# Optimization experiments

Hardware: AMD Instinct MI355X
Metric: run time of the kernel (lower is better)

Reference implementation:

```python
import jax, jax.numpy as jnp
import numpy as np

B, S, D, H = 2, 2048, 1024, 16
HEAD_DIM = D // H  # 64


def setup_inputs() -> dict:
    key = jax.random.key(0)
    ks = jax.random.split(key, 7)
    x = jax.random.normal(ks[0], (B, S, D), dtype=jnp.float32)
    W_q = jax.random.normal(ks[1], (D, D), dtype=jnp.float32) * 0.02
    W_k = jax.random.normal(ks[2], (D, D), dtype=jnp.float32) * 0.02
    W_v = jax.random.normal(ks[3], (D, D), dtype=jnp.float32) * 0.02
    W_o = jax.random.normal(ks[4], (D, D), dtype=jnp.float32) * 0.02 / np.sqrt(2 * 12)
    b_o = jnp.zeros((D,), dtype=jnp.float32)
    # Ragged prefix attention_mask: per-row valid lengths in [S/2, S];
    # row 0 forced to full length so max_valid_len == S statically (jit-safe).
    lengths = jax.random.randint(ks[5], (B,), S // 2, S + 1)
    lengths = lengths.at[0].set(S)
    attention_mask = (jnp.arange(S)[None, :] < lengths[:, None]).astype(jnp.float32)
    return {"x": x, "attention_mask": attention_mask, "W_q": W_q, "W_k": W_k,
            "W_v": W_v, "W_o": W_o, "b_o": b_o}


def reference(x, attention_mask, W_q, W_k, W_v, W_o, b_o):
    b, s, d = x.shape
    h, hd = H, HEAD_DIM
    # QKV projections (no bias, qkv_bias=False)
    q = (x @ W_q.T).reshape(b, s, h, hd).transpose(0, 2, 1, 3)  # [b,h,s,hd]
    # Masking keys/values at invalid (padded) positions; for prefix masks this
    # is exactly the module's per-batch packing loop (max_valid_len == s).
    m = attention_mask[:, None, :, None]  # [b,1,s,1]
    k = ((x @ W_k.T).reshape(b, s, h, hd).transpose(0, 2, 1, 3)) * m
    v = ((x @ W_v.T).reshape(b, s, h, hd).transpose(0, 2, 1, 3)) * m
    # Naive causal attention, same op order as the torch module:
    # mask with -inf first, then scale by 1/sqrt(head_dim), then softmax.
    causal = jnp.triu(jnp.ones((s, s), dtype=bool), 1)  # True above diagonal
    scores = jnp.einsum('bhqd,bhkd->bhqk', q, k)
    scores = jnp.where(causal[None, None], -jnp.inf, scores)
    att = jax.nn.softmax(scores / jnp.sqrt(jnp.float32(hd)), axis=-1)
    ctx = jnp.einsum('bhqk,bhkd->bhqd', att, v)  # [b,h,s,hd]
    ctx = ctx.transpose(0, 2, 1, 3).reshape(b, s, d)
    # Output projection (dropout is inference no-op)
    return ctx @ W_o.T + b_o
```

## Files before the change

### kernel.cpp

```cpp
#include <hip/hip_runtime.h>

#define B_  2
#define S_  2048
#define D_  1024
#define H_  16
#define HD_ 64
#define N3_ 3072
#define M_  4096

typedef _Float16 f16;
typedef _Float16 f16x2 __attribute__((ext_vector_type(2)));
typedef _Float16 f16x4 __attribute__((ext_vector_type(4)));
typedef _Float16 f16x8 __attribute__((ext_vector_type(8)));
typedef float    f32x4 __attribute__((ext_vector_type(4)));

__device__ __forceinline__ void async16(const f16* g, f16* l) {
  __builtin_amdgcn_global_load_lds(
      (const __attribute__((address_space(1))) unsigned int*)g,
      (__attribute__((address_space(3))) unsigned int*)l, 16, 0, 0);
}

__device__ __forceinline__ f16x2 pkrtz(float a, float b) {
  return __builtin_bit_cast(f16x2, __builtin_amdgcn_cvt_pkrtz(a, b));
}

__device__ __forceinline__ float vexp2(float x) {
  float r; asm("v_exp_f32 %0, %1" : "=v"(r) : "v"(x)); return r;
}

__global__ __launch_bounds__(256)
void cvt_all(const float* __restrict__ x,
             const float* __restrict__ Wq, const float* __restrict__ Wk,
             const float* __restrict__ Wv, const float* __restrict__ Wo,
             f16* __restrict__ xb, f16* __restrict__ wdst, float qscale) {
  const int i = blockIdx.x * 256 + threadIdx.x;
  const int XN4 = M_ * D_ / 4;
  const int WN4 = D_ * D_ / 4;
  const float* src;
  f16* dst;
  float scale = 1.0f;
  int j;
  if (i < XN4) {
    src = x; dst = xb; j = i;
  } else {
    int k = i - XN4;
    int m = k >> 18;
    j = k & (WN4 - 1);
    src = (m == 0) ? Wq : (m == 1) ? Wk : (m == 2) ? Wv : Wo;
    if (m == 0) scale = qscale;
    dst = wdst + (size_t)m * D_ * D_;
  }
  float4 v = ((const float4*)src)[j];
  f16x4 o = { (f16)(v.x * scale), (f16)(v.y * scale),
              (f16)(v.z * scale), (f16)(v.w * scale) };
  ((f16x4*)dst)[j] = o;
}

__global__ __launch_bounds__(256)
void gemm_qkv(const f16* __restrict__ A, const f16* __restrict__ Bw,
              f16* __restrict__ Cq, f16* __restrict__ vtout,
              const float* __restrict__ mask) {
  __shared__ f16 As0[64 * 64];
  __shared__ f16 Bs0[128 * 64];
  __shared__ f16 As1[64 * 64];
  __shared__ f16 Bs1[128 * 64];

  const int tid  = threadIdx.x;
  const int lane = tid & 63;
  const int w    = tid >> 6;
  const int lcol = lane & 15;
  const int quad = lane >> 4;
  const int lx   = lcol & 7;
  const int wave_m = w >> 1, wave_n = w & 1;

  const int lin  = blockIdx.x;
  const int xcd  = lin & 7;
  const int c    = lin >> 3;
  const int mIdx = c / 12;
  const int nIdx = c - mIdx * 12;
  const int m0 = ((xcd >> 1) * 16 + mIdx) * 64;
  const int n0 = ((xcd & 1) * 12 + nIdx) * 128;

  const int rr  = lane >> 3;
  const int gch = (lane & 7) ^ rr;

  const f16* gA[2];
  const f16* gB[4];
#pragma unroll
  for (int i = 0; i < 2; i++) {
    int seg = 2 * w + i;
    gA[i] = A + (size_t)(m0 + seg * 8 + rr) * D_ + gch * 8;
  }
#pragma unroll
  for (int i = 0; i < 4; i++) {
    int seg = i * 4 + w;
    gB[i] = Bw + (size_t)(n0 + seg * 8 + rr) * D_ + gch * 8;
  }

  int offA[2], offB[4];
#pragma unroll
  for (int i = 0; i < 2; i++) offA[i] = (wave_m * 32 + i * 16 + lcol) * 64;
#pragma unroll
  for (int i = 0; i < 4; i++) offB[i] = (wave_n * 64 + i * 16 + lcol) * 64;

  const f32x4 zero = {0.f, 0.f, 0.f, 0.f};
  f32x4 acc[2][4];
#pragma unroll
  for (int i = 0; i < 2; i++)
#pragma unroll
    for (int j = 0; j < 4; j++) acc[i][j] = zero;

  auto stage = [&](int k0, f16* sA, f16* sB) {
#pragma unroll
    for (int i = 0; i < 2; i++) async16(gA[i] + k0, sA + (2 * w + i) * 512);
#pragma unroll
    for (int i = 0; i < 4; i++) async16(gB[i] + k0, sB + (i * 4 + w) * 512);
  };
  auto compute = [&](const f16* sA, const f16* sB) {
#pragma unroll
    for (int ks = 0; ks < 2; ks++) {
      const int co = ((quad + 4 * ks) ^ lx) * 8;
      f16x8 af[2], bf[4];
#pragma unroll
      for (int i = 0; i < 2; i++) af[i] = *(const f16x8*)(sA + offA[i] + co);
#pragma unroll
      for (int i = 0; i < 4; i++) bf[i] = *(const f16x8*)(sB + offB[i] + co);
#pragma unroll
      for (int mi = 0; mi < 2; mi++)
#pragma unroll
        for (int ni = 0; ni < 4; ni++)
          acc[mi][ni] = __builtin_amdgcn_mfma_f32_16x16x32_f16(
              af[mi], bf[ni], acc[mi][ni], 0, 0, 0);
    }
  };

  stage(0, As0, Bs0);
  for (int it = 0; it < 14; it += 2) {
    stage((it + 1) * 64, As1, Bs1);
    asm volatile("s_waitcnt vmcnt(6)\ns_barrier" ::: "memory");
    compute(As0, Bs0);
    asm volatile("s_barrier" ::: "memory");
    stage((it + 2) * 64, As0, Bs0);
    asm volatile("s_waitcnt vmcnt(6)\ns_barrier" ::: "memory");
    compute(As1, Bs1);
    asm volatile("s_barrier" ::: "memory");
  }
  stage(15 * 64, As1, Bs1);
  asm volatile("s_waitcnt vmcnt(6)\ns_barrier" ::: "memory");
  compute(As0, Bs0);
  asm volatile("s_waitcnt vmcnt(0)\ns_barrier" ::: "memory");
  compute(As1, Bs1);

#pragma unroll
  for (int mi = 0; mi < 2; mi++) {
    const int mgb = m0 + wave_m * 32 + mi * 16 + quad * 4;
    const int bb = mgb >> 11, s = mgb & (S_ - 1);
    const float mk0 = mask[mgb], mk1 = mask[mgb + 1];
    const float mk2 = mask[mgb + 2], mk3 = mask[mgb + 3];
    const float mks[4] = {mk0, mk1, mk2, mk3};
    if (n0 >= 2 * D_) {
#pragma unroll
      for (int ni = 0; ni < 4; ni++) {
        const int vcol = n0 - 2 * D_ + wave_n * 64 + ni * 16 + lcol;
        f16x4 v = { (f16)(acc[mi][ni][0] * mk0), (f16)(acc[mi][ni][1] * mk1),
                    (f16)(acc[mi][ni][2] * mk2), (f16)(acc[mi][ni][3] * mk3) };
        *(f16x4*)(vtout +
                  ((size_t)(bb * 16 + (vcol >> 6)) * 64 + (vcol & 63)) * S_ + s) = v;
      }
    } else {
      const bool kmask = (n0 >= D_);
#pragma unroll
      for (int r = 0; r < 4; r++) {
        const float mk = kmask ? mks[r] : 1.0f;
#pragma unroll
        for (int ni = 0; ni < 4; ni++) {
          int ng = n0 + wave_n * 64 + ni * 16 + lcol;
          Cq[(size_t)(mgb + r) * N3_ + ng] = (f16)(acc[mi][ni][r] * mk);
        }
      }
    }
  }
}

__global__ __launch_bounds__(256)
void gemm_proj(const f16* __restrict__ A, const f16* __restrict__ Bw,
               float* __restrict__ Cf, const float* __restrict__ bias) {
  __shared__ f16 As0[64 * 64];
  __shared__ f16 Bs0[128 * 64];
  __shared__ f16 As1[64 * 64];
  __shared__ f16 Bs1[128 * 64];

  const int tid  = threadIdx.x;
  const int lane = tid & 63;
  const int w    = tid >> 6;
  const int lcol = lane & 15;
  const int quad = lane >> 4;
  const int lx   = lcol & 7;
  const int wave_m = w >> 1, wave_n = w & 1;

  const int lin  = blockIdx.x;
  const int xcd  = lin & 7;
  const int c    = lin >> 3;
  const int mIdx = c >> 2;
  const int nIdx = c & 3;
  const int m0 = ((xcd >> 1) * 16 + mIdx) * 64;
  const int n0 = ((xcd & 1) * 4 + nIdx) * 128;

  const int rr  = lane >> 3;
  const int gch = (lane & 7) ^ rr;

  const f16* gA[2];
  const f16* gB[4];
#pragma unroll
  for (int i = 0; i < 2; i++) {
    int seg = 2 * w + i;
    gA[i] = A + (size_t)(m0 + seg * 8 + rr) * D_ + gch * 8;
  }
#pragma unroll
  for (int i = 0; i < 4; i++) {
    int seg = i * 4 + w;
    gB[i] = Bw + (size_t)(n0 + seg * 8 + rr) * D_ + gch * 8;
  }

  int offA[2], offB[4];
#pragma unroll
  for (int i = 0; i < 2; i++) offA[i] = (wave_m * 32 + i * 16 + lcol) * 64;
#pragma unroll
  for (int i = 0; i < 4; i++) offB[i] = (wave_n * 64 + i * 16 + lcol) * 64;

  const f32x4 zero = {0.f, 0.f, 0.f, 0.f};
  f32x4 acc[2][4];
#pragma unroll
  for (int i = 0; i < 2; i++)
#pragma unroll
    for (int j = 0; j < 4; j++) acc[i][j] = zero;

  auto stage = [&](int k0, f16* sA, f16* sB) {
#pragma unroll
    for (int i = 0; i < 2; i++) async16(gA[i] + k0, sA + (2 * w + i) * 512);
#pragma unroll
    for (int i = 0; i < 4; i++) async16(gB[i] + k0, sB + (i * 4 + w) * 512);
  };
  auto compute = [&](const f16* sA, const f16* sB) {
#pragma unroll
    for (int ks = 0; ks < 2; ks++) {
      const int co = ((quad + 4 * ks) ^ lx) * 8;
      f16x8 af[2], bf[4];
#pragma unroll
      for (int i = 0; i < 2; i++) af[i] = *(const f16x8*)(sA + offA[i] + co);
#pragma unroll
      for (int i = 0; i < 4; i++) bf[i] = *(const f16x8*)(sB + offB[i] + co);
#pragma unroll
      for (int mi = 0; mi < 2; mi++)
#pragma unroll
        for (int ni = 0; ni < 4; ni++)
          acc[mi][ni] = __builtin_amdgcn_mfma_f32_16x16x32_f16(
              af[mi], bf[ni], acc[mi][ni], 0, 0, 0);
    }
  };

  stage(0, As0, Bs0);
  for (int it = 0; it < 14; it += 2) {
    stage((it + 1) * 64, As1, Bs1);
    asm volatile("s_waitcnt vmcnt(6)\ns_barrier" ::: "memory");
    compute(As0, Bs0);
    asm volatile("s_barrier" ::: "memory");
    stage((it + 2) * 64, As0, Bs0);
    asm volatile("s_waitcnt vmcnt(6)\ns_barrier" ::: "memory");
    compute(As1, Bs1);
    asm volatile("s_barrier" ::: "memory");
  }
  stage(15 * 64, As1, Bs1);
  asm volatile("s_waitcnt vmcnt(6)\ns_barrier" ::: "memory");
  compute(As0, Bs0);
  asm volatile("s_waitcnt vmcnt(0)\ns_barrier" ::: "memory");
  compute(As1, Bs1);

#pragma unroll
  for (int mi = 0; mi < 2; mi++) {
#pragma unroll
    for (int r = 0; r < 4; r++) {
      int mg = m0 + wave_m * 32 + mi * 16 + quad * 4 + r;
#pragma unroll
      for (int ni = 0; ni < 4; ni++) {
        int ng = n0 + wave_n * 64 + ni * 16 + lcol;
        Cf[(size_t)mg * D_ + ng] = acc[mi][ni][r] + bias[ng];
      }
    }
  }
}

__global__ __launch_bounds__(128)
void flash_attn8(const f16* __restrict__ qkv, const f16* __restrict__ vt,
                 f16* __restrict__ ctx, float* __restrict__ part) {
  __shared__ f16 Ks[64 * 64];
  __shared__ f16 Vs[64 * 64];

  const int tid  = threadIdx.x;
  const int lane = tid & 63;
  const int w    = tid >> 6;
  const int lcol = lane & 15;
  const int quad = lane >> 4;
  const int lx   = lcol & 7;

  const int id   = blockIdx.x;
  const int bh   = (id & 7) + 8 * ((id >> 3) & 3);
  const int u    = id >> 5;
  const int p    = u & 15;
  const int role = u >> 4;
  const int g    = 31 - p;
  const int b    = bh >> 4, h = bh & 15;

  const int rsub = lane >> 3;
  const int gch  = (lane & 7) ^ rsub;
  const f16* Kg = qkv + (size_t)b * S_ * N3_ + D_ + h * HD_;
  const f16* Vg = vt + (size_t)bh * HD_ * S_;

  int srow[4];
  f16 *ldsK[4], *ldsV[4];
#pragma unroll
  for (int i = 0; i < 4; i++) {
    const int r0 = w * 32 + i * 8;
    srow[i] = r0 + rsub;
    ldsK[i] = Ks + r0 * 64;
    ldsV[i] = Vs + r0 * 64;
  }

  const f32x4 zero = {0.f, 0.f, 0.f, 0.f};
  f32x4 o0[4], o1[4];
  float lp0, lp1;

  auto run = [&](int qt, int ktb, int kte) {
    const int qrow0 = qt * 64 + w * 32 + lcol;
    const int qrow1 = qrow0 + 16;
    const f16* Qp0 = qkv + (size_t)(b * S_ + qrow0) * N3_ + h * HD_;
    const f16* Qp1 = qkv + (size_t)(b * S_ + qrow1) * N3_ + h * HD_;
    const f16x8 qa0 = *(const f16x8*)(Qp0 + quad * 8);
    const f16x8 qa1 = *(const f16x8*)(Qp0 + 32 + quad * 8);
    const f16x8 qb0 = *(const f16x8*)(Qp1 + quad * 8);
    const f16x8 qb1 = *(const f16x8*)(Qp1 + 32 + quad * 8);
#pragma unroll
    for (int i = 0; i < 4; i++) { o0[i] = zero; o1[i] = zero; }
    lp0 = 0.f; lp1 = 0.f;

    for (int kt = ktb; kt < kte; kt++) {
      const int kbase = kt * 64;
      __syncthreads();
#pragma unroll
      for (int i = 0; i < 4; i++)
        async16(Kg + (size_t)(kbase + srow[i]) * N3_ + gch * 8, ldsK[i]);
#pragma unroll
      for (int i = 0; i < 4; i++)
        async16(Vg + (size_t)srow[i] * S_ + kbase + gch * 8, ldsV[i]);
      __syncthreads();

      f32x4 sc0[4], sc1[4];
#pragma unroll
      for (int ct = 0; ct < 4; ct++) {
        const f16* kr = Ks + (ct * 16 + lcol) * 64;
        f16x8 kf0 = *(const f16x8*)(kr + ((quad    ) ^ lx) * 8);
        f16x8 kf1 = *(const f16x8*)(kr + ((quad + 4) ^ lx) * 8);
        f32x4 z0 = zero;
        z0 = __builtin_amdgcn_mfma_f32_16x16x32_f16(kf0, qa0, z0, 0, 0, 0);
        z0 = __builtin_amdgcn_mfma_f32_16x16x32_f16(kf1, qa1, z0, 0, 0, 0);
        sc0[ct] = z0;
        f32x4 z1 = zero;
        z1 = __builtin_amdgcn_mfma_f32_16x16x32_f16(kf0, qb0, z1, 0, 0, 0);
        z1 = __builtin_amdgcn_mfma_f32_16x16x32_f16(kf1, qb1, z1, 0, 0, 0);
        sc1[ct] = z1;
      }

      if (kt == qt) {
        const int qoff0 = w * 32 + lcol;
        const int qoff1 = qoff0 + 16;
#pragma unroll
        for (int ct = 0; ct < 4; ct++) {
          const int koff = ct * 16 + quad * 4;
#pragma unroll
          for (int r = 0; r < 4; r++) {
            if (koff + r > qoff0) sc0[ct][r] = -1e30f;
            if (koff + r > qoff1) sc1[ct][r] = -1e30f;
          }
        }
      }

      f16x4 pf0[4], pf1[4];
#pragma unroll
      for (int ct = 0; ct < 4; ct++) {
        float a0 = vexp2(sc0[ct][0]), a1 = vexp2(sc0[ct][1]);
        float a2 = vexp2(sc0[ct][2]), a3 = vexp2(sc0[ct][3]);
        lp0 += (a0 + a1) + (a2 + a3);
        f16x2 alo = pkrtz(a0, a1);
        f16x2 ahi = pkrtz(a2, a3);
        f16x4 pa = { alo[0], alo[1], ahi[0], ahi[1] };
        pf0[ct] = pa;
        float b0 = vexp2(sc1[ct][0]), b1 = vexp2(sc1[ct][1]);
        float b2 = vexp2(sc1[ct][2]), b3 = vexp2(sc1[ct][3]);
        lp1 += (b0 + b1) + (b2 + b3);
        f16x2 blo = pkrtz(b0, b1);
        f16x2 bhi = pkrtz(b2, b3);
        f16x4 pb = { blo[0], blo[1], bhi[0], bhi[1] };
        pf1[ct] = pb;
      }

#pragma unroll
      for (int ht = 0; ht < 4; ht++) {
        const f16* vr = Vs + (ht * 16 + lcol) * 64 + (quad & 1) * 4;
#pragma unroll
        for (int ct = 0; ct < 4; ct++) {
          f16x4 vf = *(const f16x4*)(vr + (((2 * ct + (quad >> 1)) ^ lx) * 8));
          o0[ht] = __builtin_amdgcn_mfma_f32_16x16x16f16(vf, pf0[ct], o0[ht], 0, 0, 0);
          o1[ht] = __builtin_amdgcn_mfma_f32_16x16x16f16(vf, pf1[ct], o1[ht], 0, 0, 0);
        }
      }
    }
    lp0 += __shfl_xor(lp0, 16);
    lp0 += __shfl_xor(lp0, 32);
    lp1 += __shfl_xor(lp1, 16);
    lp1 += __shfl_xor(lp1, 32);
  };

  const int row0 = w * 32 + lcol;
  const int row1 = row0 + 16;

  if (role == 0) {
    run(g, 0, 16);
    float* slot = part + ((size_t)(bh * 16 + p) * 2 + 0) * 4160;
#pragma unroll
    for (int ht = 0; ht < 4; ht++) {
      *(f32x4*)(slot + row0 * 64 + ht * 16 + quad * 4) = o0[ht];
      *(f32x4*)(slot + row1 * 64 + ht * 16 + quad * 4) = o1[ht];
    }
    if (quad == 0) {
      slot[4096 + row0] = lp0;
      slot[4096 + row1] = lp1;
    }
  } else {
    run(g, 16, g + 1);
    float* slot = part + ((size_t)(bh * 16 + p) * 2 + 1) * 4160;
#pragma unroll
    for (int ht = 0; ht < 4; ht++) {
      *(f32x4*)(slot + row0 * 64 + ht * 16 + quad * 4) = o0[ht];
      *(f32x4*)(slot + row1 * 64 + ht * 16 + quad * 4) = o1[ht];
    }
    if (quad == 0) {
      slot[4096 + row0] = lp0;
      slot[4096 + row1] = lp1;
    }

    run(p, 0, p + 1);
    const float inv0 = 1.f / lp0;
    const float inv1 = 1.f / lp1;
    f16* cp0 = ctx + (size_t)(b * S_ + p * 64 + row0) * D_ + h * HD_ + quad * 4;
    f16* cp1 = ctx + (size_t)(b * S_ + p * 64 + row1) * D_ + h * HD_ + quad * 4;
#pragma unroll
    for (int ht = 0; ht < 4; ht++) {
      f16x4 ov0 = { (f16)(o0[ht][0] * inv0), (f16)(o0[ht][1] * inv0),
                    (f16)(o0[ht][2] * inv0), (f16)(o0[ht][3] * inv0) };
      *(f16x4*)(cp0 + ht * 16) = ov0;
      f16x4 ov1 = { (f16)(o1[ht][0] * inv1), (f16)(o1[ht][1] * inv1),
                    (f16)(o1[ht][2] * inv1), (f16)(o1[ht][3] * inv1) };
      *(f16x4*)(cp1 + ht * 16) = ov1;
    }
  }
}

__global__ __launch_bounds__(256)
void attn_combine(const float* __restrict__ part, f16* __restrict__ ctx) {
  const int sid = blockIdx.x;
  const int bh  = sid >> 4, p = sid & 15;
  const int g   = 31 - p;
  const int b   = bh >> 4, h = bh & 15;
  const int t   = threadIdx.x;
  const int row = t >> 2;
  const int c0  = (t & 3) * 16;

  const float* sA = part + ((size_t)sid * 2 + 0) * 4160;
  const float* sB = part + ((size_t)sid * 2 + 1) * 4160;
  const float inv = 1.f / (sA[4096 + row] + sB[4096 + row]);
  const int qrow = g * 64 + row;
  f16* cp = ctx + (size_t)(b * S_ + qrow) * D_ + h * HD_ + c0;
#pragma unroll
  for (int j0 = 0; j0 < 16; j0 += 4) {
    f32x4 a  = *(const f32x4*)(sA + row * 64 + c0 + j0);
    f32x4 bb = *(const f32x4*)(sB + row * 64 + c0 + j0);
    f16x4 ov = { (f16)((a[0] + bb[0]) * inv), (f16)((a[1] + bb[1]) * inv),
                 (f16)((a[2] + bb[2]) * inv), (f16)((a[3] + bb[3]) * inv) };
    *(f16x4*)(cp + j0) = ov;
  }
}

extern "C" void kernel_launch(void* const* d_in, const int* in_sizes, int n_in,
                              void* d_out, int out_size, void* d_ws, size_t ws_size,
                              hipStream_t stream) {
  (void)in_sizes; (void)n_in; (void)out_size; (void)ws_size;
  const float* x  = (const float*)d_in[0];
  const float* am = (const float*)d_in[1];
  const float* Wq = (const float*)d_in[2];
  const float* Wk = (const float*)d_in[3];
  const float* Wv = (const float*)d_in[4];
  const float* Wo = (const float*)d_in[5];
  const float* bo = (const float*)d_in[6];
  float* out = (float*)d_out;

  f16* ws   = (f16*)d_ws;
  f16* wqkv = ws;
  f16* wo16 = wqkv + (size_t)3 * D_ * D_;
  f16* xb   = wo16 + (size_t)D_ * D_;
  f16* qkvb = xb + (size_t)M_ * D_;
  f16* vtb  = qkvb + (size_t)M_ * N3_;
  f16* ctxb = vtb + (size_t)M_ * D_;
  float* part = (float*)(ctxb + (size_t)M_ * D_);

  const float qscale = 0.125f * 1.4426950408889634f;

  cvt_all<<<dim3((M_ * D_ + 4 * D_ * D_) / 1024), 256, 0, stream>>>(
      x, Wq, Wk, Wv, Wo, xb, wqkv, qscale);

  gemm_qkv<<<dim3(1536), 256, 0, stream>>>(
      xb, wqkv, qkvb, vtb, am);
  flash_attn8<<<dim3(1024), 128, 0, stream>>>(qkvb, vtb, ctxb, part);
  attn_combine<<<dim3(512), 256, 0, stream>>>(part, ctxb);
  gemm_proj<<<dim3(512), 256, 0, stream>>>(
      ctxb, wo16, out, bo);
}
```

Measured before the change: 172.9 us.

## Double-buffer K/V tiles in flash attention with async prefetch

Doubles the K and V LDS tiles and prefetches the next key tile with async global-to-LDS loads while the current tile is computed. Waits use partial vmcnt counts plus raw s_barrier instead of a full __syncthreads pair on every iteration. The aim is to hide global load latency behind MFMA and exp work. In exchange LDS use doubles to 32KB per block, which may reduce occupancy, and the hand-written waitcnt and barrier sequence is easy to get wrong.

```diff
diff --git a/kernel.cpp b/kernel.cpp
--- a/kernel.cpp
+++ b/kernel.cpp
@@ -291,10 +291,12 @@
 }
 
 __global__ __launch_bounds__(128)
-void flash_attn8(const f16* __restrict__ qkv, const f16* __restrict__ vt,
+void flash_attn9(const f16* __restrict__ qkv, const f16* __restrict__ vt,
                  f16* __restrict__ ctx, float* __restrict__ part) {
-  __shared__ f16 Ks[64 * 64];
-  __shared__ f16 Vs[64 * 64];
+  __shared__ f16 Ks0[64 * 64];
+  __shared__ f16 Vs0[64 * 64];
+  __shared__ f16 Ks1[64 * 64];
+  __shared__ f16 Vs1[64 * 64];
 
   const int tid  = threadIdx.x;
   const int lane = tid & 63;
@@ -316,103 +318,130 @@
   const f16* Kg = qkv + (size_t)b * S_ * N3_ + D_ + h * HD_;
   const f16* Vg = vt + (size_t)bh * HD_ * S_;
 
-  int srow[4];
-  f16 *ldsK[4], *ldsV[4];
+  int srow[4], lofs[4];
 #pragma unroll
   for (int i = 0; i < 4; i++) {
     const int r0 = w * 32 + i * 8;
     srow[i] = r0 + rsub;
-    ldsK[i] = Ks + r0 * 64;
-    ldsV[i] = Vs + r0 * 64;
+    lofs[i] = r0 * 64;
   }
 
   const f32x4 zero = {0.f, 0.f, 0.f, 0.f};
   f32x4 o0[4], o1[4];
   float lp0, lp1;
+  f16x8 qa0, qa1, qb0, qb1;
+
+  auto stageT = [&](int kt, f16* Kd, f16* Vd) {
+    const int kbase = kt * 64;
+#pragma unroll
+    for (int i = 0; i < 4; i++)
+      async16(Kg + (size_t)(kbase + srow[i]) * N3_ + gch * 8, Kd + lofs[i]);
+#pragma unroll
+    for (int i = 0; i < 4; i++)
+      async16(Vg + (size_t)srow[i] * S_ + kbase + gch * 8, Vd + lofs[i]);
+  };
+
+  auto computeT = [&](const f16* Kc, const f16* Vc, bool diag) {
+    f32x4 sc0[4], sc1[4];
+#pragma unroll
+    for (int ct = 0; ct < 4; ct++) {
+      const f16* kr = Kc + (ct * 16 + lcol) * 64;
+      f16x8 kf0 = *(const f16x8*)(kr + ((quad    ) ^ lx) * 8);
+      f16x8 kf1 = *(const f16x8*)(kr + ((quad + 4) ^ lx) * 8);
+      f32x4 z0 = zero;
+      z0 = __builtin_amdgcn_mfma_f32_16x16x32_f16(kf0, qa0, z0, 0, 0, 0);
+      z0 = __builtin_amdgcn_mfma_f32_16x16x32_f16(kf1, qa1, z0, 0, 0, 0);
+      sc0[ct] = z0;
+      f32x4 z1 = zero;
+      z1 = __builtin_amdgcn_mfma_f32_16x16x32_f16(kf0, qb0, z1, 0, 0, 0);
+      z1 = __builtin_amdgcn_mfma_f32_16x16x32_f16(kf1, qb1, z1, 0, 0, 0);
+      sc1[ct] = z1;
+    }
+
+    if (diag) {
+      const int qoff0 = w * 32 + lcol;
+      const int qoff1 = qoff0 + 16;
+#pragma unroll
+      for (int ct = 0; ct < 4; ct++) {
+        const int koff = ct * 16 + quad * 4;
+#pragma unroll
+        for (int r = 0; r < 4; r++) {
+          if (koff + r > qoff0) sc0[ct][r] = -1e30f;
+          if (koff + r > qoff1) sc1[ct][r] = -1e30f;
+        }
+      }
+    }
+
+    f16x4 pf0[4], pf1[4];
+#pragma unroll
+    for (int ct = 0; ct < 4; ct++) {
+      float a0 = vexp2(sc0[ct][0]), a1 = vexp2(sc0[ct][1]);
+      float a2 = vexp2(sc0[ct][2]), a3 = vexp2(sc0[ct][3]);
+      lp0 += (a0 + a1) + (a2 + a3);
+      f16x2 alo = pkrtz(a0, a1);
+      f16x2 ahi = pkrtz(a2, a3);
+      f16x4 pa = { alo[0], alo[1], ahi[0], ahi[1] };
+      pf0[ct] = pa;
+      float b0 = vexp2(sc1[ct][0]), b1 = vexp2(sc1[ct][1]);
+      float b2 = vexp2(sc1[ct][2]), b3 = vexp2(sc1[ct][3]);
+      lp1 += (b0 + b1) + (b2 + b3);
+      f16x2 blo = pkrtz(b0, b1);
+      f16x2 bhi = pkrtz(b2, b3);
+      f16x4 pb = { blo[0], blo[1], bhi[0], bhi[1] };
+      pf1[ct] = pb;
+    }
+
+#pragma unroll
+    for (int ht = 0; ht < 4; ht++) {
+      const f16* vr = Vc + (ht * 16 + lcol) * 64 + (quad & 1) * 4;
+#pragma unroll
+      for (int ct = 0; ct < 4; ct++) {
+        f16x4 vf = *(const f16x4*)(vr + (((2 * ct + (quad >> 1)) ^ lx) * 8));
+        o0[ht] = __builtin_amdgcn_mfma_f32_16x16x16f16(vf, pf0[ct], o0[ht], 0, 0, 0);
+        o1[ht] = __builtin_amdgcn_mfma_f32_16x16x16f16(vf, pf1[ct], o1[ht], 0, 0, 0);
+      }
+    }
+  };
 
   auto run = [&](int qt, int ktb, int kte) {
     const int qrow0 = qt * 64 + w * 32 + lcol;
     const int qrow1 = qrow0 + 16;
     const f16* Qp0 = qkv + (size_t)(b * S_ + qrow0) * N3_ + h * HD_;
     const f16* Qp1 = qkv + (size_t)(b * S_ + qrow1) * N3_ + h * HD_;
-    const f16x8 qa0 = *(const f16x8*)(Qp0 + quad * 8);
-    const f16x8 qa1 = *(const f16x8*)(Qp0 + 32 + quad * 8);
-    const f16x8 qb0 = *(const f16x8*)(Qp1 + quad * 8);
-    const f16x8 qb1 = *(const f16x8*)(Qp1 + 32 + quad * 8);
+    qa0 = *(const f16x8*)(Qp0 + quad * 8);
+    qa1 = *(const f16x8*)(Qp0 + 32 + quad * 8);
+    qb0 = *(const f16x8*)(Qp1 + quad * 8);
+    qb1 = *(const f16x8*)(Qp1 + 32 + quad * 8);
 #pragma unroll
     for (int i = 0; i < 4; i++) { o0[i] = zero; o1[i] = zero; }
     lp0 = 0.f; lp1 = 0.f;
 
-    for (int kt = ktb; kt < kte; kt++) {
-      const int kbase = kt * 64;
-      __syncthreads();
-#pragma unroll
-      for (int i = 0; i < 4; i++)
-        async16(Kg + (size_t)(kbase + srow[i]) * N3_ + gch * 8, ldsK[i]);
-#pragma unroll
-      for (int i = 0; i < 4; i++)
-        async16(Vg + (size_t)srow[i] * S_ + kbase + gch * 8, ldsV[i]);
-      __syncthreads();
-
-      f32x4 sc0[4], sc1[4];
-#pragma unroll
-      for (int ct = 0; ct < 4; ct++) {
-        const f16* kr = Ks + (ct * 16 + lcol) * 64;
-        f16x8 kf0 = *(const f16x8*)(kr + ((quad    ) ^ lx) * 8);
-        f16x8 kf1 = *(const f16x8*)(kr + ((quad + 4) ^ lx) * 8);
-        f32x4 z0 = zero;
-        z0 = __builtin_amdgcn_mfma_f32_16x16x32_f16(kf0, qa0, z0, 0, 0, 0);
-        z0 = __builtin_amdgcn_mfma_f32_16x16x32_f16(kf1, qa1, z0, 0, 0, 0);
-        sc0[ct] = z0;
-        f32x4 z1 = zero;
-        z1 = __builtin_amdgcn_mfma_f32_16x16x32_f16(kf0, qb0, z1, 0, 0, 0);
-        z1 = __builtin_amdgcn_mfma_f32_16x16x32_f16(kf1, qb1, z1, 0, 0, 0);
-        sc1[ct] = z1;
-      }
-
-      if (kt == qt) {
-        const int qoff0 = w * 32 + lcol;
-        const int qoff1 = qoff0 + 16;
-#pragma unroll
-        for (int ct = 0; ct < 4; ct++) {
-          const int koff = ct * 16 + quad * 4;
-#pragma unroll
-          for (int r = 0; r < 4; r++) {
-            if (koff + r > qoff0) sc0[ct][r] = -1e30f;
-            if (koff + r > qoff1) sc1[ct][r] = -1e30f;
-          }
+    __syncthreads();
+
+    stageT(ktb, Ks0, Vs0);
+    int kt = ktb;
+    while (kt < kte) {
+      const bool h1 = (kt + 1 < kte);
+      if (h1) {
+        stageT(kt + 1, Ks1, Vs1);
+        asm volatile("s_waitcnt vmcnt(8)\ns_barrier" ::: "memory");
+      } else {
+        asm volatile("s_waitcnt vmcnt(0)\ns_barrier" ::: "memory");
+      }
+      computeT(Ks0, Vs0, kt == qt);
+      asm volatile("s_barrier" ::: "memory");
+      if (h1) {
+        const bool h2 = (kt + 2 < kte);
+        if (h2) {
+          stageT(kt + 2, Ks0, Vs0);
+          asm volatile("s_waitcnt vmcnt(8)\ns_barrier" ::: "memory");
+        } else {
+          asm volatile("s_waitcnt vmcnt(0)\ns_barrier" ::: "memory");
         }
-      }
-
-      f16x4 pf0[4], pf1[4];
-#pragma unroll
-      for (int ct = 0; ct < 4; ct++) {
-        float a0 = vexp2(sc0[ct][0]), a1 = vexp2(sc0[ct][1]);
-        float a2 = vexp2(sc0[ct][2]), a3 = vexp2(sc0[ct][3]);
-        lp0 += (a0 + a1) + (a2 + a3);
-        f16x2 alo = pkrtz(a0, a1);
-        f16x2 ahi = pkrtz(a2, a3);
-        f16x4 pa = { alo[0], alo[1], ahi[0], ahi[1] };
-        pf0[ct] = pa;
-        float b0 = vexp2(sc1[ct][0]), b1 = vexp2(sc1[ct][1]);
-        float b2 = vexp2(sc1[ct][2]), b3 = vexp2(sc1[ct][3]);
-        lp1 += (b0 + b1) + (b2 + b3);
-        f16x2 blo = pkrtz(b0, b1);
-        f16x2 bhi = pkrtz(b2, b3);
-        f16x4 pb = { blo[0], blo[1], bhi[0], bhi[1] };
-        pf1[ct] = pb;
-      }
-
-#pragma unroll
-      for (int ht = 0; ht < 4; ht++) {
-        const f16* vr = Vs + (ht * 16 + lcol) * 64 + (quad & 1) * 4;
-#pragma unroll
-        for (int ct = 0; ct < 4; ct++) {
-          f16x4 vf = *(const f16x4*)(vr + (((2 * ct + (quad >> 1)) ^ lx) * 8));
-          o0[ht] = __builtin_amdgcn_mfma_f32_16x16x16f16(vf, pf0[ct], o0[ht], 0, 0, 0);
-          o1[ht] = __builtin_amdgcn_mfma_f32_16x16x16f16(vf, pf1[ct], o1[ht], 0, 0, 0);
-        }
-      }
+        computeT(Ks1, Vs1, kt + 1 == qt);
+        asm volatile("s_barrier" ::: "memory");
+      }
+      kt += 2;
     }
     lp0 += __shfl_xor(lp0, 16);
     lp0 += __shfl_xor(lp0, 32);
@@ -519,7 +548,7 @@
 
   gemm_qkv<<<dim3(1536), 256, 0, stream>>>(
       xb, wqkv, qkvb, vtb, am);
-  flash_attn8<<<dim3(1024), 128, 0, stream>>>(qkvb, vtb, ctxb, part);
+  flash_attn9<<<dim3(1024), 128, 0, stream>>>(qkvb, vtb, ctxb, part);
   attn_combine<<<dim3(512), 256, 0, stream>>>(part, ctxb);
   gemm_proj<<<dim3(512), 256, 0, stream>>>(
       ctxb, wo16, out, bo);
```

Result: no change. 173.8 us (+0.5%).

## Fuse split-KV partial combine into output projection GEMM A-tile loading

Applied to the files above, without the earlier changes.

Removes the separate attn_combine kernel. For row blocks in the second half of each sequence, where flash attention wrote split partial results, gemm_proj now reads the two fp32 partials and their row sums, normalizes them, converts to fp16 and writes the swizzled A tile into LDS directly. This drops one launch and a ctx round trip through memory. The fused path is single-buffered with full syncthreads per k-step, so it loses the async double-buffered overlap for those blocks and adds load imbalance between block types.

```diff
diff --git a/kernel.cpp b/kernel.cpp
--- a/kernel.cpp
+++ b/kernel.cpp
@@ -184,7 +184,8 @@
 
 __global__ __launch_bounds__(256)
 void gemm_proj(const f16* __restrict__ A, const f16* __restrict__ Bw,
-               float* __restrict__ Cf, const float* __restrict__ bias) {
+               float* __restrict__ Cf, const float* __restrict__ bias,
+               const float* __restrict__ part) {
   __shared__ f16 As0[64 * 64];
   __shared__ f16 Bs0[128 * 64];
   __shared__ f16 As1[64 * 64];
@@ -259,22 +260,68 @@
     }
   };
 
-  stage(0, As0, Bs0);
-  for (int it = 0; it < 14; it += 2) {
-    stage((it + 1) * 64, As1, Bs1);
+  const bool bigA = ((m0 & (S_ - 1)) >= 1024);
+
+  if (!bigA) {
+    stage(0, As0, Bs0);
+    for (int it = 0; it < 14; it += 2) {
+      stage((it + 1) * 64, As1, Bs1);
+      asm volatile("s_waitcnt vmcnt(6)\ns_barrier" ::: "memory");
+      compute(As0, Bs0);
+      asm volatile("s_barrier" ::: "memory");
+      stage((it + 2) * 64, As0, Bs0);
+      asm volatile("s_waitcnt vmcnt(6)\ns_barrier" ::: "memory");
+      compute(As1, Bs1);
+      asm volatile("s_barrier" ::: "memory");
+    }
+    stage(15 * 64, As1, Bs1);
     asm volatile("s_waitcnt vmcnt(6)\ns_barrier" ::: "memory");
     compute(As0, Bs0);
-    asm volatile("s_barrier" ::: "memory");
-    stage((it + 2) * 64, As0, Bs0);
-    asm volatile("s_waitcnt vmcnt(6)\ns_barrier" ::: "memory");
+    asm volatile("s_waitcnt vmcnt(0)\ns_barrier" ::: "memory");
     compute(As1, Bs1);
-    asm volatile("s_barrier" ::: "memory");
-  }
-  stage(15 * 64, As1, Bs1);
-  asm volatile("s_waitcnt vmcnt(6)\ns_barrier" ::: "memory");
-  compute(As0, Bs0);
-  asm volatile("s_waitcnt vmcnt(0)\ns_barrier" ::: "memory");
-  compute(As1, Bs1);
+  } else {
+    const int bb = m0 >> 11;
+    const int g  = (m0 & (S_ - 1)) >> 6;
+    const int p  = 31 - g;
+    const int r  = tid >> 2;
+    const int c16 = (tid & 3) * 16;
+    const int ch0 = (tid & 3) * 2;
+    const int rx  = r & 7;
+
+    for (int k0 = 0; k0 < D_; k0 += 64) {
+      const int h = k0 >> 6;
+      const float* sA = part + ((size_t)((bb * 16 + h) * 16 + p) * 2 + 0) * 4160;
+      const float* sB = sA + 4160;
+
+      __syncthreads();
+#pragma unroll
+      for (int i = 0; i < 4; i++) async16(gB[i] + k0, Bs0 + (i * 4 + w) * 512);
+
+      const float inv = 1.f / (sA[4096 + r] + sB[4096 + r]);
+      f32x4 va[4], vb[4];
+#pragma unroll
+      for (int j = 0; j < 4; j++) {
+        va[j] = *(const f32x4*)(sA + r * 64 + c16 + j * 4);
+        vb[j] = *(const f32x4*)(sB + r * 64 + c16 + j * 4);
+      }
+      f16x8 lo, hi;
+#pragma unroll
+      for (int j = 0; j < 2; j++)
+#pragma unroll
+        for (int e = 0; e < 4; e++)
+          lo[j * 4 + e] = (f16)((va[j][e] + vb[j][e]) * inv);
+#pragma unroll
+      for (int j = 0; j < 2; j++)
+#pragma unroll
+        for (int e = 0; e < 4; e++)
+          hi[j * 4 + e] = (f16)((va[2 + j][e] + vb[2 + j][e]) * inv);
+      *(f16x8*)(As0 + r * 64 + ((ch0 ^ rx)) * 8)       = lo;
+      *(f16x8*)(As0 + r * 64 + (((ch0 + 1) ^ rx)) * 8) = hi;
+
+      __syncthreads();
+      compute(As0, Bs0);
+    }
+  }
 
 #pragma unroll
   for (int mi = 0; mi < 2; mi++) {
@@ -465,31 +512,6 @@
   }
 }
 
-__global__ __launch_bounds__(256)
-void attn_combine(const float* __restrict__ part, f16* __restrict__ ctx) {
-  const int sid = blockIdx.x;
-  const int bh  = sid >> 4, p = sid & 15;
-  const int g   = 31 - p;
-  const int b   = bh >> 4, h = bh & 15;
-  const int t   = threadIdx.x;
-  const int row = t >> 2;
-  const int c0  = (t & 3) * 16;
-
-  const float* sA = part + ((size_t)sid * 2 + 0) * 4160;
-  const float* sB = part + ((size_t)sid * 2 + 1) * 4160;
-  const float inv = 1.f / (sA[4096 + row] + sB[4096 + row]);
-  const int qrow = g * 64 + row;
-  f16* cp = ctx + (size_t)(b * S_ + qrow) * D_ + h * HD_ + c0;
-#pragma unroll
-  for (int j0 = 0; j0 < 16; j0 += 4) {
-    f32x4 a  = *(const f32x4*)(sA + row * 64 + c0 + j0);
-    f32x4 bb = *(const f32x4*)(sB + row * 64 + c0 + j0);
-    f16x4 ov = { (f16)((a[0] + bb[0]) * inv), (f16)((a[1] + bb[1]) * inv),
-                 (f16)((a[2] + bb[2]) * inv), (f16)((a[3] + bb[3]) * inv) };
-    *(f16x4*)(cp + j0) = ov;
-  }
-}
-
 extern "C" void kernel_launch(void* const* d_in, const int* in_sizes, int n_in,
                               void* d_out, int out_size, void* d_ws, size_t ws_size,
                               hipStream_t stream) {
@@ -520,7 +542,6 @@
   gemm_qkv<<<dim3(1536), 256, 0, stream>>>(
       xb, wqkv, qkvb, vtb, am);
   flash_attn8<<<dim3(1024), 128, 0, stream>>>(qkvb, vtb, ctxb, part);
-  attn_combine<<<dim3(512), 256, 0, stream>>>(part, ctxb);
   gemm_proj<<<dim3(512), 256, 0, stream>>>(
-      ctxb, wo16, out, bo);
-}
+      ctxb, wo16, out, bo, part);
+}
```

Result: slower. 183.6 us (+6.2%).

## Triple-buffer QKV GEMM LDS staging to prefetch two k-tiles ahead

Applied to the files above, without the earlier changes.

Adds a third LDS buffer pair to the QKV projection GEMM so async global-to-LDS loads run two k-steps ahead of compute instead of one. The waitcnt thresholds change so each step waits only for the oldest stage. This aims to hide more global load latency, but LDS use rises from 48KB to 72KB per block, which may reduce occupancy.

```diff
diff --git a/kernel.cpp b/kernel.cpp
--- a/kernel.cpp
+++ b/kernel.cpp
@@ -64,6 +64,8 @@
   __shared__ f16 Bs0[128 * 64];
   __shared__ f16 As1[64 * 64];
   __shared__ f16 Bs1[128 * 64];
+  __shared__ f16 As2[64 * 64];
+  __shared__ f16 Bs2[128 * 64];
 
   const int tid  = threadIdx.x;
   const int lane = tid & 63;
@@ -135,21 +137,37 @@
   };
 
   stage(0, As0, Bs0);
-  for (int it = 0; it < 14; it += 2) {
-    stage((it + 1) * 64, As1, Bs1);
-    asm volatile("s_waitcnt vmcnt(6)\ns_barrier" ::: "memory");
-    compute(As0, Bs0);
-    asm volatile("s_barrier" ::: "memory");
-    stage((it + 2) * 64, As0, Bs0);
-    asm volatile("s_waitcnt vmcnt(6)\ns_barrier" ::: "memory");
-    compute(As1, Bs1);
-    asm volatile("s_barrier" ::: "memory");
-  }
-  stage(15 * 64, As1, Bs1);
-  asm volatile("s_waitcnt vmcnt(6)\ns_barrier" ::: "memory");
-  compute(As0, Bs0);
-  asm volatile("s_waitcnt vmcnt(0)\ns_barrier" ::: "memory");
-  compute(As1, Bs1);
+  stage(64, As1, Bs1);
+#define QKV_STEP(T, CA, CB, NA, NB)                                          \
+  do {                                                                       \
+    if ((T) + 2 < 16) {                                                      \
+      stage(((T) + 2) * 64, NA, NB);                                         \
+      asm volatile("s_waitcnt vmcnt(12)\ns_barrier" ::: "memory");           \
+    } else if ((T) + 1 < 16) {                                               \
+      asm volatile("s_waitcnt vmcnt(6)\ns_barrier" ::: "memory");            \
+    } else {                                                                 \
+      asm volatile("s_waitcnt vmcnt(0)\ns_barrier" ::: "memory");            \
+    }                                                                        \
+    compute(CA, CB);                                                         \
+    asm volatile("s_barrier" ::: "memory");                                  \
+  } while (0)
+  QKV_STEP(0,  As0, Bs0, As2, Bs2);
+  QKV_STEP(1,  As1, Bs1, As0, Bs0);
+  QKV_STEP(2,  As2, Bs2, As1, Bs1);
+  QKV_STEP(3,  As0, Bs0, As2, Bs2);
+  QKV_STEP(4,  As1, Bs1, As0, Bs0);
+  QKV_STEP(5,  As2, Bs2, As1, Bs1);
+  QKV_STEP(6,  As0, Bs0, As2, Bs2);
+  QKV_STEP(7,  As1, Bs1, As0, Bs0);
+  QKV_STEP(8,  As2, Bs2, As1, Bs1);
+  QKV_STEP(9,  As0, Bs0, As2, Bs2);
+  QKV_STEP(10, As1, Bs1, As0, Bs0);
+  QKV_STEP(11, As2, Bs2, As1, Bs1);
+  QKV_STEP(12, As0, Bs0, As2, Bs2);
+  QKV_STEP(13, As1, Bs1, As0, Bs0);
+  QKV_STEP(14, As2, Bs2, As0, Bs0);
+  QKV_STEP(15, As0, Bs0, As1, Bs1);
+#undef QKV_STEP
 
 #pragma unroll
   for (int mi = 0; mi < 2; mi++) {
```

Result: slower. 178.4 us (+3.2%).
